# Performance work log

Hardware: AMD Instinct MI355X
Metric: run time of the kernel (lower is better)

Reference implementation:

```python
import jax, jax.numpy as jnp
import numpy as np

# Config (matches init_kwargs)
L = 2        # depth
DIM = 512
H = 8        # heads
DH = 64      # dim_head
MLP = 2048
B = 4
N = 1024
BLOCK = 32   # compress / selection block size
TOPK = 8     # num_selected_blocks
WRAD = 32    # sliding window radius (window size 64)


def setup_inputs() -> dict:
    key = jax.random.key(0)
    ks = jax.random.split(key, 10)
    s = 0.02
    def rn(k, shape):
        return jax.random.normal(k, shape, dtype=jnp.float32) * s
    return {
        "x": jax.random.normal(ks[0], (B, N, DIM), dtype=jnp.float32),
        "ln1_g": jnp.ones((L, DIM), jnp.float32), "ln1_b": jnp.zeros((L, DIM), jnp.float32),
        "Wq": rn(ks[1], (L, DIM, H * DH)), "Wk": rn(ks[2], (L, DIM, H * DH)), "Wv": rn(ks[3], (L, DIM, H * DH)),
        "Wg": rn(ks[4], (L, DIM, H * 3)), "bg": jnp.zeros((L, H * 3), jnp.float32),
        "Wo": rn(ks[5], (L, H * DH, DIM)), "bo": jnp.zeros((L, DIM), jnp.float32),
        "ln2_g": jnp.ones((L, DIM), jnp.float32), "ln2_b": jnp.zeros((L, DIM), jnp.float32),
        "W1": rn(ks[6], (L, DIM, MLP)), "b1": jnp.zeros((L, MLP), jnp.float32),
        "W2": rn(ks[7], (L, MLP, DIM)), "b2": jnp.zeros((L, DIM), jnp.float32),
    }


def _ln(x, g, b):
    m = x.mean(-1, keepdims=True)
    v = jnp.var(x, axis=-1, keepdims=True)
    return (x - m) * jax.lax.rsqrt(v + 1e-5) * g + b


def _sparse_attn(x, lng, lnb, Wq, Wk, Wv, Wg, bg, Wo, bo):
    # NSA-style 3-branch attention: compressed + selected-blocks + sliding window,
    # combined with per-head sigmoid gates. Non-causal (ViT).
    b, n, _ = x.shape
    h = _ln(x, lng, lnb)
    q = (h @ Wq).reshape(b, n, H, DH).transpose(0, 2, 1, 3)  # bhnd
    k = (h @ Wk).reshape(b, n, H, DH).transpose(0, 2, 1, 3)
    v = (h @ Wv).reshape(b, n, H, DH).transpose(0, 2, 1, 3)
    q = q * (DH ** -0.5)
    nb = n // BLOCK
    # --- compressed branch: mean-pool K/V per block
    kc = k.reshape(b, H, nb, BLOCK, DH).mean(3)              # bhmd (m = nb blocks)
    vc = v.reshape(b, H, nb, BLOCK, DH).mean(3)
    sc = jnp.einsum('bhnd,bhmd->bhnm', q, kc)                # per-query block scores
    out_c = jnp.einsum('bhnm,bhmd->bhnd', jax.nn.softmax(sc, -1), vc)
    # --- selection branch: top-k blocks per query (from compressed scores)
    idx = jax.lax.top_k(sc, TOPK)[1]                         # [b,h,n,TOPK]
    blk_mask = (idx[..., :, None] == jnp.arange(nb)).any(-2) # [b,h,n,nb]
    tok_mask = jnp.repeat(blk_mask, BLOCK, axis=-1)          # [b,h,n,n]
    s = jnp.einsum('bhnd,bhmd->bhnm', q, k)                  # shared fine scores
    neg = jnp.finfo(s.dtype).min
    out_s = jnp.einsum('bhnm,bhmd->bhnd',
                       jax.nn.softmax(jnp.where(tok_mask, s, neg), -1), v)
    # --- sliding window branch
    i = jnp.arange(n)
    wmask = jnp.abs(i[:, None] - i[None, :]) <= WRAD
    out_w = jnp.einsum('bhnm,bhmd->bhnd',
                       jax.nn.softmax(jnp.where(wmask, s, neg), -1), v)
    # --- gate and combine
    gates = jax.nn.sigmoid(h @ Wg + bg).reshape(b, n, H, 3).transpose(0, 2, 1, 3)[..., None]  # [b,H,n,3,1]
    out = gates[:, :, :, 0] * out_c + gates[:, :, :, 1] * out_s + gates[:, :, :, 2] * out_w
    out = out.transpose(0, 2, 1, 3).reshape(b, n, H * DH)
    return out @ Wo + bo


def reference(x, ln1_g, ln1_b, Wq, Wk, Wv, Wg, bg, Wo, bo, ln2_g, ln2_b, W1, b1, W2, b2):
    for l in range(L):
        x = _sparse_attn(x, ln1_g[l], ln1_b[l], Wq[l], Wk[l], Wv[l],
                         Wg[l], bg[l], Wo[l], bo[l]) + x
        h = _ln(x, ln2_g[l], ln2_b[l])
        x = jax.nn.gelu(h @ W1[l] + b1[l]) @ W2[l] + b2[l] + x
    return x
```

## Files before the change

### kernel.cpp

```cpp
#include <hip/hip_runtime.h>
#include <cstdint>
#include <cstddef>

typedef __attribute__((ext_vector_type(4))) float f32x4;
typedef __attribute__((ext_vector_type(16))) float f32x16;
typedef __attribute__((ext_vector_type(8))) short short8;
typedef __attribute__((ext_vector_type(4))) short s16x4;
typedef __attribute__((ext_vector_type(2))) int int2v;
typedef unsigned short u16;

#define DEVINL static __device__ __forceinline__
#define MFMA32(A,B,C) __builtin_amdgcn_mfma_f32_32x32x16_bf16(A,B,C,0,0,0)

constexpr int NBATCH = 4;
constexpr int NSEQ   = 1024;
constexpr int NDIM   = 512;
constexpr int NHEAD  = 8;
constexpr int NDH    = 64;
constexpr int NMLP   = 2048;
constexpr int NROWS  = NBATCH * NSEQ;
constexpr int NBLKC  = 32;
constexpr int NBH    = NBATCH * NHEAD;
constexpr int NQKV   = 1664;

DEVINL float b2f(u16 u) { union { unsigned u; float f; } x; x.u = ((unsigned)u) << 16; return x.f; }
DEVINL u16 f2b(float v) {
    union { float f; unsigned u; } x; x.f = v;
    unsigned r = x.u + 0x7fff + ((x.u >> 16) & 1);
    return (u16)(r >> 16);
}
DEVINL float fastrcp(float x) { float r; asm("v_rcp_f32 %0, %1" : "=v"(r) : "v"(x)); return r; }

DEVINL void gload16(const void* g, void* l)
{
    __builtin_amdgcn_global_load_lds(
        (const __attribute__((address_space(1))) void*)g,
        (__attribute__((address_space(3))) void*)l, 16, 0, 0);
}

__global__ void __launch_bounds__(256) ln_kernel(const float* __restrict__ x,
    const float* __restrict__ gg, const float* __restrict__ bb, u16* __restrict__ out)
{
    int row = blockIdx.x * 4 + (threadIdx.x >> 6);
    int lane = threadIdx.x & 63;
    const float* xr = x + (size_t)row * NDIM + lane * 8;
    f32x4 a = *(const f32x4*)xr;
    f32x4 c = *(const f32x4*)(xr + 4);
    float xv[8] = { a[0], a[1], a[2], a[3], c[0], c[1], c[2], c[3] };
    float s = 0.f, s2 = 0.f;
    #pragma unroll
    for (int i = 0; i < 8; ++i) { s += xv[i]; s2 += xv[i] * xv[i]; }
    #pragma unroll
    for (int d = 1; d < 64; d <<= 1) { s += __shfl_xor(s, d); s2 += __shfl_xor(s2, d); }
    float mean = s * (1.f / NDIM);
    float var = s2 * (1.f / NDIM) - mean * mean;
    float rstd = rsqrtf(var + 1e-5f);
    const float* gp = gg + lane * 8;
    const float* bp = bb + lane * 8;
    short8 o;
    #pragma unroll
    for (int i = 0; i < 8; ++i)
        o[i] = (short)f2b((xv[i] - mean) * rstd * gp[i] + bp[i]);
    *(short8*)(out + (size_t)row * NDIM + lane * 8) = o;
}

__global__ void __launch_bounds__(256) transpose_w(const float* __restrict__ W,
    u16* __restrict__ WT, int K, int Nc, size_t sstr, size_t dstr)
{
    W  += (size_t)blockIdx.z * sstr;
    WT += (size_t)blockIdx.z * dstr;
    __shared__ float tile[32][33];
    int tx = threadIdx.x & 31;
    int ty = threadIdx.x >> 5;
    int n0 = blockIdx.x * 32, k0 = blockIdx.y * 32;
    #pragma unroll
    for (int r = 0; r < 4; ++r) {
        int kr = ty * 4 + r;
        tile[kr][tx] = W[(size_t)(k0 + kr) * Nc + n0 + tx];
    }
    __syncthreads();
    #pragma unroll
    for (int r = 0; r < 4; ++r) {
        int nr = ty * 4 + r;
        WT[(size_t)(n0 + nr) * K + k0 + tx] = f2b(tile[tx][nr]);
    }
}

__global__ void __launch_bounds__(256) transpose_qkv(const float* __restrict__ Wq,
    const float* __restrict__ Wk, const float* __restrict__ Wv, u16* __restrict__ WT)
{
    int z = blockIdx.z;
    int l = z / 3, w = z % 3;
    const float* W = (w == 0 ? Wq : (w == 1 ? Wk : Wv)) + (size_t)l * 262144;
    u16* dst = WT + (size_t)l * NQKV * 512 + (size_t)w * 512 * 512;
    __shared__ float tile[32][33];
    int tx = threadIdx.x & 31;
    int ty = threadIdx.x >> 5;
    int n0 = blockIdx.x * 32, k0 = blockIdx.y * 32;
    #pragma unroll
    for (int r = 0; r < 4; ++r) {
        int kr = ty * 4 + r;
        tile[kr][tx] = W[(size_t)(k0 + kr) * 512 + n0 + tx];
    }
    __syncthreads();
    #pragma unroll
    for (int r = 0; r < 4; ++r) {
        int nr = ty * 4 + r;
        dst[(size_t)(n0 + nr) * 512 + k0 + tx] = f2b(tile[tx][nr]);
    }
}

__global__ void __launch_bounds__(256) fill_wg(const float* __restrict__ Wg, u16* __restrict__ WT)
{
    int l = blockIdx.x, r = blockIdx.y;
    u16* dst = WT + (size_t)l * NQKV * 512 + (size_t)(1536 + r) * 512;
    const float* src = Wg + (size_t)l * 512 * 24;
    for (int k = threadIdx.x; k < 512; k += 256)
        dst[k] = (r < 24) ? f2b(src[(size_t)k * 24 + r]) : (u16)0;
}

__global__ void __launch_bounds__(256) pool_kernel(const u16* __restrict__ kb,
    const u16* __restrict__ vt, u16* __restrict__ kc16, u16* __restrict__ vct16)
{
    int idx = blockIdx.x * 256 + threadIdx.x;
    int d = idx & 63, m = (idx >> 6) & 31, bh = idx >> 11;
    const u16* kp = kb + ((size_t)bh * NSEQ + m * 32) * NDH + d;
    float sk = 0.f;
    #pragma unroll 8
    for (int j = 0; j < 32; ++j) sk += b2f(kp[j * NDH]);
    const u16* vp = vt + (size_t)bh * 65536 + (size_t)d * NSEQ + m * 32;
    float sv = 0.f;
    #pragma unroll 8
    for (int j = 0; j < 32; ++j) sv += b2f(vp[j]);
    kc16[(size_t)bh * 2048 + m * 64 + d] = f2b(sk * (1.f / 32.f));
    vct16[(size_t)bh * 2048 + d * 32 + m] = f2b(sv * (1.f / 32.f));
}

enum { EP_QKV = 0, EP_GELU = 1, EP_RES = 2 };

template<int BM, int BN, int BK, int KT, int EPIL>
__global__ void __launch_bounds__(256) gemm_k(
    const u16* __restrict__ A, const u16* __restrict__ BT,
    int M, int Nc,
    const float* __restrict__ bias,
    float* __restrict__ resout,
    u16* __restrict__ outb,
    u16* __restrict__ q16, u16* __restrict__ k16, u16* __restrict__ vt16)
{
    constexpr int NT = KT / BK;
    constexpr int NK = BK / 32;
    constexpr int RB = BK * 2;
    constexpr int RMSK = (BK == 64) ? 7 : 3;
    constexpr int LA = BM * BK / 2048;
    constexpr int LBD = BN * BK / 2048;
    constexpr int LB = LA + LBD;
    constexpr int WM = BM / 2, WN = BN / 2;
    constexpr int MI = WM / 16, NI = WN / 16;
    __shared__ u16 As[3][BM][BK];
    __shared__ u16 Bs[3][BN][BK];
    const int tid = threadIdx.x;
    const int lane = tid & 63;
    const int wid = tid >> 6;
    const int wm = wid >> 1, wn = wid & 1;
    const int gx = gridDim.x;
    const int nblk = gx * gridDim.y;
    const int id = blockIdx.y * gx + blockIdx.x;
    const int sid = (id & 7) * (nblk >> 3) + (id >> 3);
    const int rowBase = (sid / gx) * BM;
    const int colBase = (sid % gx) * BN;
    const int fr = lane & 15;
    const int kg = lane >> 4;

    auto stage = [&](int buf, int t) {
        const size_t k0 = (size_t)t * BK;
        char* aL = (char*)&As[buf][0][0];
        #pragma unroll
        for (int p = 0; p < LA; ++p) {
            int idx = p * 256 + tid;
            int row = idx / (BK / 8);
            int ob = (idx % (BK / 8)) * 16;
            int sw = ob ^ ((row & RMSK) << 4);
            gload16((const char*)(A + (size_t)(rowBase + row) * KT + k0) + sw, aL + idx * 16);
        }
        char* bL = (char*)&Bs[buf][0][0];
        #pragma unroll
        for (int p = 0; p < LBD; ++p) {
            int idx = p * 256 + tid;
            int row = idx / (BK / 8);
            int ob = (idx % (BK / 8)) * 16;
            int sw = ob ^ ((row & RMSK) << 4);
            gload16((const char*)(BT + (size_t)(colBase + row) * KT + k0) + sw, bL + idx * 16);
        }
    };

    stage(0, 0);
    stage(1, 1);
    f32x4 acc[MI][NI] = {};
    int cb = 0, nb = 1, sb = 2;
    for (int t = 0; t < NT; ++t) {
        if (t == NT - 1) asm volatile("s_waitcnt vmcnt(0)" ::: "memory");
        else             asm volatile("s_waitcnt vmcnt(%0)" :: "n"(LB) : "memory");
        __builtin_amdgcn_s_barrier();
        if (t + 2 < NT) stage(sb, t + 2);
        const char* aB = (const char*)&As[cb][0][0];
        const char* bB = (const char*)&Bs[cb][0][0];
        #pragma unroll
        for (int kk = 0; kk < NK; ++kk) {
            short8 af[MI], bfr[NI];
            #pragma unroll
            for (int i = 0; i < MI; ++i) {
                int row = wm * WM + i * 16 + fr;
                af[i] = *(const short8*)(aB + row * RB + ((kk * 64 + kg * 16) ^ ((row & RMSK) << 4)));
            }
            #pragma unroll
            for (int j = 0; j < NI; ++j) {
                int row = wn * WN + j * 16 + fr;
                bfr[j] = *(const short8*)(bB + row * RB + ((kk * 64 + kg * 16) ^ ((row & RMSK) << 4)));
            }
            #pragma unroll
            for (int i = 0; i < MI; ++i)
                #pragma unroll
                for (int j = 0; j < NI; ++j)
                    acc[i][j] = __builtin_amdgcn_mfma_f32_16x16x32_bf16(af[i], bfr[j], acc[i][j], 0, 0, 0);
        }
        int tmp = cb; cb = nb; nb = sb; sb = tmp;
    }

    #pragma unroll
    for (int i = 0; i < MI; ++i) {
        #pragma unroll
        for (int j = 0; j < NI; ++j) {
            int col = colBase + wn * WN + j * 16 + fr;
            if constexpr (EPIL == EP_QKV) {
                int which = col >> 9;
                int row0 = rowBase + wm * WM + i * 16 + kg * 4;
                if (which >= 3) {
                    int c2 = col - 1536;
                    if (c2 < 24) {
                        #pragma unroll
                        for (int rr = 0; rr < 4; ++rr) {
                            float xg = acc[i][j][rr] + bias[c2];
                            resout[(size_t)(row0 + rr) * 24 + c2] =
                                fastrcp(1.f + exp2f(-1.4426950409f * xg));
                        }
                    }
                } else {
                    int c = col & 511;
                    int hh = c >> 6, dh = c & 63;
                    int bb2 = row0 >> 10, n0 = row0 & 1023;
                    size_t bh2 = (size_t)(bb2 * NHEAD + hh) * 65536;
                    if (which == 2) {
                        s16x4 pk;
                        #pragma unroll
                        for (int rr = 0; rr < 4; ++rr) pk[rr] = (short)f2b(acc[i][j][rr]);
                        *(s16x4*)&vt16[bh2 + (size_t)dh * NSEQ + n0] = pk;
                    } else {
                        u16* dst = (which ? k16 : q16) + bh2 + (size_t)n0 * NDH + dh;
                        float scl = which ? 1.f : 0.18033688f;
                        #pragma unroll
                        for (int rr = 0; rr < 4; ++rr) dst[rr * NDH] = f2b(acc[i][j][rr] * scl);
                    }
                }
            } else {
                #pragma unroll
                for (int rr = 0; rr < 4; ++rr) {
                    int row = rowBase + wm * WM + i * 16 + kg * 4 + rr;
                    float val = acc[i][j][rr];
                    if constexpr (EPIL == EP_GELU) {
                        float t = val + bias[col];
                        float u = t + 0.044715f * t * t * t;
                        float gs = fastrcp(1.f + exp2f(-2.3022083f * u));
                        outb[(size_t)row * Nc + col] = f2b(t * gs);
                    } else {
                        resout[(size_t)row * Nc + col] += val + bias[col];
                    }
                }
            }
        }
    }
}

DEVINL unsigned cvtpk(float lo, float hi_)
{
    unsigned t;
    asm("v_cvt_pk_bf16_f32 %0, %1, %2" : "=v"(t) : "v"(lo), "v"(hi_));
    return t;
}

DEVINL void plswap(unsigned& a, unsigned& b)
{
#if __has_builtin(__builtin_amdgcn_permlane32_swap)
    int2v r = __builtin_amdgcn_permlane32_swap((int)a, (int)b, false, false);
    a = (unsigned)r[0]; b = (unsigned)r[1];
#else
    asm("v_permlane32_swap_b32 %0, %1" : "+v"(a), "+v"(b));
#endif
}

DEVINL void packswap(const float* e, unsigned selmask, short8& pb0, short8& pb1)
{
    unsigned w[8];
    #pragma unroll
    for (int i = 0; i < 8; ++i) w[i] = cvtpk(e[2 * i], e[2 * i + 1]) & selmask;
    plswap(w[0], w[2]); plswap(w[1], w[3]);
    plswap(w[4], w[6]); plswap(w[5], w[7]);
    union { unsigned u[4]; short8 s; } c0, c1;
    c0.u[0] = w[0]; c0.u[1] = w[1]; c0.u[2] = w[2]; c0.u[3] = w[3];
    c1.u[0] = w[4]; c1.u[1] = w[5]; c1.u[2] = w[6]; c1.u[3] = w[7];
    pb0 = c0.s; pb1 = c1.s;
}

template<int R0>
DEVINL unsigned rank4(const f32x16& sc_, const float* po, int hi)
{
    unsigned bits = 0;
    #pragma unroll
    for (int k = 0; k < 4; ++k) {
        const int r = R0 + k;
        const int krr = (r & 3) + 8 * (r >> 2);
        const float sr = sc_[r];
        int cnt = 0;
        #pragma unroll
        for (int j = 0; j < 16; ++j) {
            const int krj = (j & 3) + 8 * (j >> 2);
            if (j != r) cnt += (sc_[j] > sr || (sc_[j] == sr && krj < krr)) ? 1 : 0;
            const bool pless = (hi == 0) ? (krj + 4 < krr) : (krj < krr + 4);
            cnt += (po[j] > sr || (po[j] == sr && pless)) ? 1 : 0;
        }
        if (cnt < 8) bits |= 1u << (krr + 4 * hi);
    }
    return bits;
}

__global__ void __launch_bounds__(256, 2) attn_mfma(
    const u16* __restrict__ qb, const u16* __restrict__ kb, const u16* __restrict__ vt,
    const u16* __restrict__ kc16, const u16* __restrict__ vct16,
    const float* __restrict__ gates, u16* __restrict__ att)
{
    __shared__ __align__(16) char smem[65536];
    unsigned* selb_lds = (unsigned*)(smem + 32768);
    const int tid = threadIdx.x;
    const int wid = tid >> 6;
    const int lane = tid & 63;
    const int qc = lane & 31, hi = lane >> 5;
    const int g = blockIdx.x;
    const int xcd = g & 7, ii = g >> 3;
    const int bh = xcd * 4 + (ii >> 5);
    const int qt = ii & 31;
    const int qrow = qt * 32 + qc;
    if (tid < 32) selb_lds[tid] = 0u;
    const u16* Q = qb + (size_t)bh * 65536;
    const char* Kby = (const char*)(kb + (size_t)bh * 65536);
    const char* Vby = (const char*)(vt + (size_t)bh * 65536);

    const int l16 = lane * 16;
    auto stage = [&](int buf, int blk) {
        char* base = smem + buf * 32768 + wid * 4096;
        #pragma unroll
        for (int i = 0; i < 4; ++i) {
            int o = i * 1024 + l16;
            int so = o ^ (((o >> 7) & 7) << 4);
            gload16(Kby + (size_t)blk * 4096 + so, base + o);
        }
        #pragma unroll
        for (int i = 0; i < 4; ++i) {
            int o = i * 1024 + l16;
            int row = o >> 6;
            int colb = (o & 63) ^ ((row & 3) << 4);
            gload16(Vby + (size_t)row * 2048 + blk * 64 + colb, base + 16384 + o);
        }
    };
    const int blo = wid * 8;
    stage(0, blo);

    short8 qf[4];
    #pragma unroll
    for (int ks = 0; ks < 4; ++ks)
        qf[ks] = *(const short8*)&Q[(size_t)qrow * 64 + ks * 16 + hi * 8];
    const int b = bh >> 3, h = bh & 7;
    const float* grow = gates + (size_t)(b * 1024 + qrow) * 24 + h * 3;
    const float g0 = grow[0], g1 = grow[1], g2 = grow[2];

    const u16* Kc = kc16 + (size_t)bh * 2048;
    const u16* Vc = vct16 + (size_t)bh * 2048;
    f32x16 sc_ = {};
    #pragma unroll
    for (int ks = 0; ks < 4; ++ks) {
        short8 kcf = *(const short8*)&Kc[qc * 64 + ks * 16 + hi * 8];
        sc_ = MFMA32(kcf, qf[ks], sc_);
    }
    float po[16];
    #pragma unroll
    for (int r = 0; r < 16; ++r) po[r] = __shfl_xor(sc_[r], 32);
    unsigned bits;
    switch (wid) {
        case 0:  bits = rank4<0>(sc_, po, hi); break;
        case 1:  bits = rank4<4>(sc_, po, hi); break;
        case 2:  bits = rank4<8>(sc_, po, hi); break;
        default: bits = rank4<12>(sc_, po, hi); break;
    }
    __syncthreads();
    atomicOr(&selb_lds[qc], bits);

    f32x16 aC = {};
    float denc = 1.f;
    if (wid < 2) {
        float ec[16]; float dsum = 0.f;
        #pragma unroll
        for (int r = 0; r < 16; ++r) { ec[r] = exp2f(sc_[r]); dsum += ec[r]; }
        denc = dsum + __shfl_xor(dsum, 32);
        short8 pc0, pc1;
        packswap(ec, 0xFFFFFFFFu, pc0, pc1);
        const u16* Vch = Vc + (wid * 32 + qc) * 32 + hi * 8;
        short8 vcA = *(const short8*)&Vch[0];
        short8 vcB = *(const short8*)&Vch[16];
        aC = MFMA32(vcA, pc0, aC);
        aC = MFMA32(vcB, pc1, aC);
    }
    __syncthreads();
    const unsigned mask = selb_lds[qc];

    f32x16 aS0 = {}, aS1 = {}, aW0 = {}, aW1 = {};
    float denS = 0.f, denW = 0.f;
    const int wlo = qt > 0 ? qt - 1 : 0;
    const int whi = qt < 31 ? qt + 1 : 31;

    int kra[4];
    #pragma unroll
    for (int ks = 0; ks < 4; ++ks)
        kra[ks] = wid * 4096 + ((qc * 128 + ks * 32 + hi * 16) ^ ((qc & 7) << 4));
    const int vbase = wid * 4096 + 16384;
    const int v00o = vbase + ((qc * 64 + hi * 16) ^ ((qc & 3) << 4));
    const int v01o = vbase + ((qc * 64 + 32 + hi * 16) ^ ((qc & 3) << 4));
    const int v10o = vbase + ((2048 + qc * 64 + hi * 16) ^ ((qc & 3) << 4));
    const int v11o = vbase + ((2048 + qc * 64 + 32 + hi * 16) ^ ((qc & 3) << 4));

    for (int t = 0; t < 8; ++t) {
        const int blk = blo + t;
        const char* base = smem + (t & 1) * 32768;
        if (t < 7) {
            stage((t + 1) & 1, blk + 1);
            asm volatile("s_waitcnt vmcnt(8)" ::: "memory");
        } else {
            asm volatile("s_waitcnt vmcnt(0)" ::: "memory");
        }
        short8 kf[4];
        #pragma unroll
        for (int ks = 0; ks < 4; ++ks)
            kf[ks] = *(const short8*)(base + kra[ks]);
        __builtin_amdgcn_s_setprio(1);
        f32x16 s = {};
        #pragma unroll
        for (int ks = 0; ks < 4; ++ks)
            s = MFMA32(kf[ks], qf[ks], s);
        __builtin_amdgcn_s_setprio(0);
        float e[16];
        #pragma unroll
        for (int r = 0; r < 16; ++r) e[r] = exp2f(s[r]);

        short8 v00 = *(const short8*)(base + v00o);
        short8 v01 = *(const short8*)(base + v01o);
        short8 v10 = *(const short8*)(base + v10o);
        short8 v11 = *(const short8*)(base + v11o);

        const bool selb = (mask >> blk) & 1u;
        const unsigned selm = selb ? 0xFFFFFFFFu : 0u;
        {
            float tt = 0.f;
            #pragma unroll
            for (int r = 0; r < 16; ++r) tt += e[r];
            denS += selb ? tt : 0.f;
        }
        short8 pb0, pb1;
        packswap(e, selm, pb0, pb1);
        __builtin_amdgcn_s_setprio(1);
        aS0 = MFMA32(v00, pb0, aS0);
        aS0 = MFMA32(v01, pb1, aS0);
        aS1 = MFMA32(v10, pb0, aS1);
        aS1 = MFMA32(v11, pb1, aS1);
        __builtin_amdgcn_s_setprio(0);

        if (blk >= wlo && blk <= whi) {
            float ew[16];
            float tt = 0.f;
            #pragma unroll
            for (int r = 0; r < 16; ++r) {
                int kr = (r & 3) + 8 * (r >> 2) + 4 * hi;
                int dd = blk * 32 + kr - qrow;
                ew[r] = (dd >= -32 && dd <= 32) ? e[r] : 0.f;
                tt += ew[r];
            }
            denW += tt;
            short8 pw0, pw1;
            packswap(ew, 0xFFFFFFFFu, pw0, pw1);
            aW0 = MFMA32(v00, pw0, aW0);
            aW0 = MFMA32(v01, pw1, aW0);
            aW1 = MFMA32(v10, pw0, aW1);
            aW1 = MFMA32(v11, pw1, aW1);
        }
    }
    __syncthreads();

    float* cmb = (float*)smem;
    if (wid > 0) {
        float* dst = cmb + (size_t)(wid - 1) * (64 * 85) + lane * 85;
        #pragma unroll
        for (int i = 0; i < 16; ++i) { dst[i] = aS0[i]; dst[16 + i] = aS1[i]; }
        #pragma unroll
        for (int i = 0; i < 16; ++i) { dst[32 + i] = aW0[i]; dst[48 + i] = aW1[i]; }
        dst[64] = denS; dst[65] = denW;
        if (wid == 1) {
            #pragma unroll
            for (int i = 0; i < 16; ++i) dst[66 + i] = aC[i];
        }
    }
    __syncthreads();
    if (wid == 0) {
        #pragma unroll
        for (int w = 1; w < 4; ++w) {
            const float* src = cmb + (size_t)(w - 1) * (64 * 85) + lane * 85;
            #pragma unroll
            for (int i = 0; i < 16; ++i) { aS0[i] += src[i]; aS1[i] += src[16 + i]; }
            #pragma unroll
            for (int i = 0; i < 16; ++i) { aW0[i] += src[32 + i]; aW1[i] += src[48 + i]; }
            denS += src[64]; denW += src[65];
        }
        f32x16 aC1;
        const float* s1 = cmb + lane * 85;
        #pragma unroll
        for (int i = 0; i < 16; ++i) aC1[i] = s1[66 + i];
        denS += __shfl_xor(denS, 32);
        denW += __shfl_xor(denW, 32);
        const float rc = g0 / denc, rs = g1 / denS, rw = g2 / denW;
        u16* op = att + (size_t)(b * 1024 + qrow) * NDIM + h * 64;
        #pragma unroll
        for (int c4 = 0; c4 < 4; ++c4) {
            int d0 = c4 * 8 + hi * 4;
            s16x4 w0, w1;
            #pragma unroll
            for (int j = 0; j < 4; ++j) {
                w0[j] = (short)f2b(rc * aC[c4 * 4 + j]  + rs * aS0[c4 * 4 + j] + rw * aW0[c4 * 4 + j]);
                w1[j] = (short)f2b(rc * aC1[c4 * 4 + j] + rs * aS1[c4 * 4 + j] + rw * aW1[c4 * 4 + j]);
            }
            *(s16x4*)&op[d0] = w0;
            *(s16x4*)&op[d0 + 32] = w1;
        }
    }
}

extern "C" void kernel_launch(void* const* d_in, const int* in_sizes, int n_in,
                              void* d_out, int out_size, void* d_ws, size_t ws_size,
                              hipStream_t stream)
{
    const float* x0    = (const float*)d_in[0];
    const float* ln1_g = (const float*)d_in[1];
    const float* ln1_b = (const float*)d_in[2];
    const float* Wq    = (const float*)d_in[3];
    const float* Wk    = (const float*)d_in[4];
    const float* Wv    = (const float*)d_in[5];
    const float* Wg    = (const float*)d_in[6];
    const float* bg    = (const float*)d_in[7];
    const float* Wo    = (const float*)d_in[8];
    const float* bo    = (const float*)d_in[9];
    const float* ln2_g = (const float*)d_in[10];
    const float* ln2_b = (const float*)d_in[11];
    const float* W1    = (const float*)d_in[12];
    const float* b1    = (const float*)d_in[13];
    const float* W2    = (const float*)d_in[14];
    const float* b2    = (const float*)d_in[15];
    float* xo = (float*)d_out;

    char* w = (char*)d_ws;
    auto alloc = [&](size_t bytes) { char* p = w; w += (bytes + 255) & ~(size_t)255; return p; };
    u16*   hbf   = (u16*)  alloc((size_t)NROWS * NDIM * 2);
    u16*   qb    = (u16*)  alloc((size_t)NBH * NSEQ * NDH * 2);
    u16*   kb    = (u16*)  alloc((size_t)NBH * NSEQ * NDH * 2);
    u16*   vt    = (u16*)  alloc((size_t)NBH * NDH * NSEQ * 2);
    u16*   att   = (u16*)  alloc((size_t)NROWS * NDIM * 2);
    float* gates = (float*)alloc((size_t)NROWS * NHEAD * 3 * 4);
    u16*   kc16  = (u16*)  alloc((size_t)NBH * NBLKC * NDH * 2);
    u16*   vct16 = (u16*)  alloc((size_t)NBH * NDH * NBLKC * 2);
    u16*   wqkvT = (u16*)  alloc((size_t)2 * NQKV * 512 * 2);
    u16*   woT   = (u16*)  alloc((size_t)2 * 512 * 512 * 2);
    u16*   w1T   = (u16*)  alloc((size_t)2 * 2048 * 512 * 2);
    u16*   w2T   = (u16*)  alloc((size_t)2 * 512 * 2048 * 2);
    u16*   mid   = (u16*)qb;

    hipMemcpyAsync(xo, x0, (size_t)NROWS * NDIM * 4, hipMemcpyDeviceToDevice, stream);

    transpose_qkv<<<dim3(16, 16, 6), 256, 0, stream>>>(Wq, Wk, Wv, wqkvT);
    fill_wg<<<dim3(2, 128), 256, 0, stream>>>(Wg, wqkvT);
    transpose_w<<<dim3(16, 16, 2), 256, 0, stream>>>(Wo, woT, 512, 512,  262144, 262144);
    transpose_w<<<dim3(64, 16, 2), 256, 0, stream>>>(W1, w1T, 512, 2048, 1048576, 1048576);
    transpose_w<<<dim3(16, 64, 2), 256, 0, stream>>>(W2, w2T, 2048, 512, 1048576, 1048576);

    for (int l = 0; l < 2; ++l) {
        ln_kernel<<<NROWS / 4, 256, 0, stream>>>(xo, ln1_g + l * NDIM, ln1_b + l * NDIM, hbf);
        gemm_k<64, 128, 64, 512, EP_QKV><<<dim3(NQKV / 128, NROWS / 64), 256, 0, stream>>>(
            hbf, wqkvT + (size_t)l * NQKV * 512, NROWS, NQKV,
            bg + l * 24, gates, nullptr, qb, kb, vt);
        pool_kernel<<<(NBH * NBLKC * NDH) / 256, 256, 0, stream>>>(kb, vt, kc16, vct16);
        attn_mfma<<<1024, 256, 0, stream>>>(qb, kb, vt, kc16, vct16, gates, att);
        gemm_k<64, 64, 64, 512, EP_RES><<<dim3(512 / 64, NROWS / 64), 256, 0, stream>>>(
            att, woT + (size_t)l * 512 * 512, NROWS, 512,
            bo + l * NDIM, xo, nullptr, nullptr, nullptr, nullptr);
        ln_kernel<<<NROWS / 4, 256, 0, stream>>>(xo, ln2_g + l * NDIM, ln2_b + l * NDIM, hbf);
        gemm_k<64, 128, 64, 512, EP_GELU><<<dim3(2048 / 128, NROWS / 64), 256, 0, stream>>>(
            hbf, w1T + (size_t)l * 2048 * 512, NROWS, 2048,
            b1 + l * NMLP, nullptr, mid, nullptr, nullptr, nullptr);
        gemm_k<64, 64, 64, 2048, EP_RES><<<dim3(512 / 64, NROWS / 64), 256, 0, stream>>>(
            mid, w2T + (size_t)l * 512 * 2048, NROWS, 512,
            b2 + l * NDIM, xo, nullptr, nullptr, nullptr, nullptr);
    }
}
```

Measured before the change: 246.8 us.

## Merge weight-prep kernels and restructure attention for higher occupancy with smaller LDS

Folds the five weight transpose/fill launches into one setup_weights kernel to cut launch overhead. The attention kernel halves its LDS (single-buffered staging) and raises launch bounds to 4 blocks per CU. The sliding-window branch moves to its own per-wave stage, and the compressed-score MFMA is recomputed later rather than kept live. The cross-wave reduction is now serialized through a swizzled LDS buffer, which adds barriers and gives up the double-buffered load/compute overlap in exchange for occupancy.

```diff
diff --git a/kernel.cpp b/kernel.cpp
--- a/kernel.cpp
+++ b/kernel.cpp
@@ -64,59 +64,53 @@
     *(short8*)(out + (size_t)row * NDIM + lane * 8) = o;
 }
 
-__global__ void __launch_bounds__(256) transpose_w(const float* __restrict__ W,
-    u16* __restrict__ WT, int K, int Nc, size_t sstr, size_t dstr)
-{
-    W  += (size_t)blockIdx.z * sstr;
-    WT += (size_t)blockIdx.z * dstr;
+__global__ void __launch_bounds__(256) setup_weights(
+    const float* __restrict__ Wq, const float* __restrict__ Wk, const float* __restrict__ Wv,
+    const float* __restrict__ Wg, const float* __restrict__ Wo,
+    const float* __restrict__ W1, const float* __restrict__ W2,
+    u16* __restrict__ wqkvT, u16* __restrict__ woT,
+    u16* __restrict__ w1T, u16* __restrict__ w2T)
+{
+    int j = blockIdx.x;
+    if (j >= 6144) {
+        int j5 = j - 6144, l = j5 >> 2, chunk = j5 & 3;
+        u16* d2 = wqkvT + (size_t)l * NQKV * 512 + (size_t)(1536 + chunk * 32) * 512;
+        const float* src = Wg + (size_t)l * 512 * 24;
+        for (int e = threadIdx.x; e < 16384; e += 256) {
+            int r = chunk * 32 + (e >> 9), k = e & 511;
+            d2[(size_t)(e >> 9) * 512 + k] = (r < 24) ? f2b(src[(size_t)k * 24 + r]) : (u16)0;
+        }
+        return;
+    }
     __shared__ float tile[32][33];
-    int tx = threadIdx.x & 31;
-    int ty = threadIdx.x >> 5;
-    int n0 = blockIdx.x * 32, k0 = blockIdx.y * 32;
-    #pragma unroll
-    for (int r = 0; r < 4; ++r) {
-        int kr = ty * 4 + r;
-        tile[kr][tx] = W[(size_t)(k0 + kr) * Nc + n0 + tx];
-    }
+    const float* W; u16* dst; int K, Nc, bx, by;
+    if (j < 1536) {
+        int z = j >> 8, t = j & 255, l = z / 3, wsel = z % 3;
+        W = (wsel == 0 ? Wq : (wsel == 1 ? Wk : Wv)) + (size_t)l * 262144;
+        dst = wqkvT + (size_t)l * NQKV * 512 + (size_t)wsel * 262144;
+        K = 512; Nc = 512; bx = t & 15; by = t >> 4;
+    } else if (j < 2048) {
+        int j2 = j - 1536, z = j2 >> 8, t = j2 & 255;
+        W = Wo + (size_t)z * 262144; dst = woT + (size_t)z * 262144;
+        K = 512; Nc = 512; bx = t & 15; by = t >> 4;
+    } else if (j < 4096) {
+        int j3 = j - 2048, z = j3 >> 10, t = j3 & 1023;
+        W = W1 + (size_t)z * 1048576; dst = w1T + (size_t)z * 1048576;
+        K = 512; Nc = 2048; bx = t & 63; by = t >> 6;
+    } else {
+        int j4 = j - 4096, z = j4 >> 10, t = j4 & 1023;
+        W = W2 + (size_t)z * 1048576; dst = w2T + (size_t)z * 1048576;
+        K = 2048; Nc = 512; bx = t & 15; by = t >> 4;
+    }
+    int tx = threadIdx.x & 31, ty = threadIdx.x >> 5;
+    int n0 = bx * 32, k0 = by * 32;
+    #pragma unroll
+    for (int r = 0; r < 4; ++r)
+        tile[ty * 4 + r][tx] = W[(size_t)(k0 + ty * 4 + r) * Nc + n0 + tx];
     __syncthreads();
     #pragma unroll
-    for (int r = 0; r < 4; ++r) {
-        int nr = ty * 4 + r;
-        WT[(size_t)(n0 + nr) * K + k0 + tx] = f2b(tile[tx][nr]);
-    }
-}
-
-__global__ void __launch_bounds__(256) transpose_qkv(const float* __restrict__ Wq,
-    const float* __restrict__ Wk, const float* __restrict__ Wv, u16* __restrict__ WT)
-{
-    int z = blockIdx.z;
-    int l = z / 3, w = z % 3;
-    const float* W = (w == 0 ? Wq : (w == 1 ? Wk : Wv)) + (size_t)l * 262144;
-    u16* dst = WT + (size_t)l * NQKV * 512 + (size_t)w * 512 * 512;
-    __shared__ float tile[32][33];
-    int tx = threadIdx.x & 31;
-    int ty = threadIdx.x >> 5;
-    int n0 = blockIdx.x * 32, k0 = blockIdx.y * 32;
-    #pragma unroll
-    for (int r = 0; r < 4; ++r) {
-        int kr = ty * 4 + r;
-        tile[kr][tx] = W[(size_t)(k0 + kr) * 512 + n0 + tx];
-    }
-    __syncthreads();
-    #pragma unroll
-    for (int r = 0; r < 4; ++r) {
-        int nr = ty * 4 + r;
-        dst[(size_t)(n0 + nr) * 512 + k0 + tx] = f2b(tile[tx][nr]);
-    }
-}
-
-__global__ void __launch_bounds__(256) fill_wg(const float* __restrict__ Wg, u16* __restrict__ WT)
-{
-    int l = blockIdx.x, r = blockIdx.y;
-    u16* dst = WT + (size_t)l * NQKV * 512 + (size_t)(1536 + r) * 512;
-    const float* src = Wg + (size_t)l * 512 * 24;
-    for (int k = threadIdx.x; k < 512; k += 256)
-        dst[k] = (r < 24) ? f2b(src[(size_t)k * 24 + r]) : (u16)0;
+    for (int r = 0; r < 4; ++r)
+        dst[(size_t)(n0 + ty * 4 + r) * K + k0 + tx] = f2b(tile[tx][ty * 4 + r]);
 }
 
 __global__ void __launch_bounds__(256) pool_kernel(const u16* __restrict__ kb,
@@ -332,17 +326,18 @@
     return bits;
 }
 
-__global__ void __launch_bounds__(256, 2) attn_mfma(
+__global__ void __launch_bounds__(256, 4) attn_mfma(
     const u16* __restrict__ qb, const u16* __restrict__ kb, const u16* __restrict__ vt,
     const u16* __restrict__ kc16, const u16* __restrict__ vct16,
     const float* __restrict__ gates, u16* __restrict__ att)
 {
-    __shared__ __align__(16) char smem[65536];
-    unsigned* selb_lds = (unsigned*)(smem + 32768);
+    __shared__ __align__(16) char smem[32768];
+    __shared__ unsigned selb_lds[32];
     const int tid = threadIdx.x;
     const int wid = tid >> 6;
     const int lane = tid & 63;
     const int qc = lane & 31, hi = lane >> 5;
+    const int lm = lane & 31;
     const int g = blockIdx.x;
     const int xcd = g & 7, ii = g >> 3;
     const int bh = xcd * 4 + (ii >> 5);
@@ -354,8 +349,8 @@
     const char* Vby = (const char*)(vt + (size_t)bh * 65536);
 
     const int l16 = lane * 16;
-    auto stage = [&](int buf, int blk) {
-        char* base = smem + buf * 32768 + wid * 4096;
+    auto stage = [&](int blk) {
+        char* base = smem + wid * 8192;
         #pragma unroll
         for (int i = 0; i < 4; ++i) {
             int o = i * 1024 + l16;
@@ -367,11 +362,11 @@
             int o = i * 1024 + l16;
             int row = o >> 6;
             int colb = (o & 63) ^ ((row & 3) << 4);
-            gload16(Vby + (size_t)row * 2048 + blk * 64 + colb, base + 16384 + o);
+            gload16(Vby + (size_t)row * 2048 + blk * 64 + colb, base + 4096 + o);
         }
     };
     const int blo = wid * 8;
-    stage(0, blo);
+    stage(blo);
 
     short8 qf[4];
     #pragma unroll
@@ -383,31 +378,134 @@
 
     const u16* Kc = kc16 + (size_t)bh * 2048;
     const u16* Vc = vct16 + (size_t)bh * 2048;
-    f32x16 sc_ = {};
-    #pragma unroll
-    for (int ks = 0; ks < 4; ++ks) {
-        short8 kcf = *(const short8*)&Kc[qc * 64 + ks * 16 + hi * 8];
-        sc_ = MFMA32(kcf, qf[ks], sc_);
-    }
-    float po[16];
-    #pragma unroll
-    for (int r = 0; r < 16; ++r) po[r] = __shfl_xor(sc_[r], 32);
-    unsigned bits;
-    switch (wid) {
-        case 0:  bits = rank4<0>(sc_, po, hi); break;
-        case 1:  bits = rank4<4>(sc_, po, hi); break;
-        case 2:  bits = rank4<8>(sc_, po, hi); break;
-        default: bits = rank4<12>(sc_, po, hi); break;
-    }
-    __syncthreads();
-    atomicOr(&selb_lds[qc], bits);
+    {
+        f32x16 sc_ = {};
+        #pragma unroll
+        for (int ks = 0; ks < 4; ++ks) {
+            short8 kcf = *(const short8*)&Kc[qc * 64 + ks * 16 + hi * 8];
+            sc_ = MFMA32(kcf, qf[ks], sc_);
+        }
+        float po[16];
+        #pragma unroll
+        for (int r = 0; r < 16; ++r) po[r] = __shfl_xor(sc_[r], 32);
+        unsigned bits;
+        switch (wid) {
+            case 0:  bits = rank4<0>(sc_, po, hi); break;
+            case 1:  bits = rank4<4>(sc_, po, hi); break;
+            case 2:  bits = rank4<8>(sc_, po, hi); break;
+            default: bits = rank4<12>(sc_, po, hi); break;
+        }
+        __syncthreads();
+        atomicOr(&selb_lds[qc], bits);
+        __syncthreads();
+    }
+    const unsigned mask = selb_lds[qc];
+
+    int kra[4];
+    #pragma unroll
+    for (int ks = 0; ks < 4; ++ks)
+        kra[ks] = wid * 8192 + ((qc * 128 + ks * 32 + hi * 16) ^ ((qc & 7) << 4));
+    const int vbase = wid * 8192 + 4096;
+    const int v00o = vbase + ((qc * 64 + hi * 16) ^ ((qc & 3) << 4));
+    const int v01o = vbase + ((qc * 64 + 32 + hi * 16) ^ ((qc & 3) << 4));
+    const int v10o = vbase + ((2048 + qc * 64 + hi * 16) ^ ((qc & 3) << 4));
+    const int v11o = vbase + ((2048 + qc * 64 + 32 + hi * 16) ^ ((qc & 3) << 4));
+    const char* base = smem;
+
+    f32x16 aS0 = {}, aS1 = {};
+    float denS = 0.f;
+    for (int t = 0; t < 8; ++t) {
+        const int blk = blo + t;
+        asm volatile("s_waitcnt vmcnt(0)" ::: "memory");
+        short8 kf[4];
+        #pragma unroll
+        for (int ks = 0; ks < 4; ++ks)
+            kf[ks] = *(const short8*)(base + kra[ks]);
+        short8 v00 = *(const short8*)(base + v00o);
+        short8 v01 = *(const short8*)(base + v01o);
+        short8 v10 = *(const short8*)(base + v10o);
+        short8 v11 = *(const short8*)(base + v11o);
+        if (t < 7) {
+            asm volatile("s_waitcnt lgkmcnt(0)" ::: "memory");
+            stage(blk + 1);
+        }
+        __builtin_amdgcn_s_setprio(1);
+        f32x16 s = {};
+        #pragma unroll
+        for (int ks = 0; ks < 4; ++ks)
+            s = MFMA32(kf[ks], qf[ks], s);
+        __builtin_amdgcn_s_setprio(0);
+        float e[16];
+        #pragma unroll
+        for (int r = 0; r < 16; ++r) e[r] = exp2f(s[r]);
+        const bool selb = (mask >> blk) & 1u;
+        const unsigned selm = selb ? 0xFFFFFFFFu : 0u;
+        {
+            float tt = 0.f;
+            #pragma unroll
+            for (int r = 0; r < 16; ++r) tt += e[r];
+            denS += selb ? tt : 0.f;
+        }
+        short8 pb0, pb1;
+        packswap(e, selm, pb0, pb1);
+        __builtin_amdgcn_s_setprio(1);
+        aS0 = MFMA32(v00, pb0, aS0);
+        aS0 = MFMA32(v01, pb1, aS0);
+        aS1 = MFMA32(v10, pb0, aS1);
+        aS1 = MFMA32(v11, pb1, aS1);
+        __builtin_amdgcn_s_setprio(0);
+    }
+
+    f32x16 aW0 = {}, aW1 = {};
+    float denW = 0.f;
+    const int wblk = qt - 1 + wid;
+    if (wid < 3 && wblk >= 0 && wblk <= 31) {
+        asm volatile("s_waitcnt lgkmcnt(0)" ::: "memory");
+        stage(wblk);
+        asm volatile("s_waitcnt vmcnt(0)" ::: "memory");
+        short8 kf[4];
+        #pragma unroll
+        for (int ks = 0; ks < 4; ++ks)
+            kf[ks] = *(const short8*)(base + kra[ks]);
+        short8 v00 = *(const short8*)(base + v00o);
+        short8 v01 = *(const short8*)(base + v01o);
+        short8 v10 = *(const short8*)(base + v10o);
+        short8 v11 = *(const short8*)(base + v11o);
+        f32x16 s = {};
+        #pragma unroll
+        for (int ks = 0; ks < 4; ++ks)
+            s = MFMA32(kf[ks], qf[ks], s);
+        float ew[16];
+        float tt = 0.f;
+        #pragma unroll
+        for (int r = 0; r < 16; ++r) {
+            int kr = (r & 3) + 8 * (r >> 2) + 4 * hi;
+            int dd = wblk * 32 + kr - qrow;
+            float ev = exp2f(s[r]);
+            ew[r] = (dd >= -32 && dd <= 32) ? ev : 0.f;
+            tt += ew[r];
+        }
+        denW += tt;
+        short8 pw0, pw1;
+        packswap(ew, 0xFFFFFFFFu, pw0, pw1);
+        aW0 = MFMA32(v00, pw0, aW0);
+        aW0 = MFMA32(v01, pw1, aW0);
+        aW1 = MFMA32(v10, pw0, aW1);
+        aW1 = MFMA32(v11, pw1, aW1);
+    }
 
     f32x16 aC = {};
     float denc = 1.f;
     if (wid < 2) {
+        f32x16 sc2 = {};
+        #pragma unroll
+        for (int ks = 0; ks < 4; ++ks) {
+            short8 kcf = *(const short8*)&Kc[qc * 64 + ks * 16 + hi * 8];
+            sc2 = MFMA32(kcf, qf[ks], sc2);
+        }
         float ec[16]; float dsum = 0.f;
         #pragma unroll
-        for (int r = 0; r < 16; ++r) { ec[r] = exp2f(sc_[r]); dsum += ec[r]; }
+        for (int r = 0; r < 16; ++r) { ec[r] = exp2f(sc2[r]); dsum += ec[r]; }
         denc = dsum + __shfl_xor(dsum, 32);
         short8 pc0, pc1;
         packswap(ec, 0xFFFFFFFFu, pc0, pc1);
@@ -417,118 +515,48 @@
         aC = MFMA32(vcA, pc0, aC);
         aC = MFMA32(vcB, pc1, aC);
     }
+
     __syncthreads();
-    const unsigned mask = selb_lds[qc];
-
-    f32x16 aS0 = {}, aS1 = {}, aW0 = {}, aW1 = {};
-    float denS = 0.f, denW = 0.f;
-    const int wlo = qt > 0 ? qt - 1 : 0;
-    const int whi = qt < 31 ? qt + 1 : 31;
-
-    int kra[4];
-    #pragma unroll
-    for (int ks = 0; ks < 4; ++ks)
-        kra[ks] = wid * 4096 + ((qc * 128 + ks * 32 + hi * 16) ^ ((qc & 7) << 4));
-    const int vbase = wid * 4096 + 16384;
-    const int v00o = vbase + ((qc * 64 + hi * 16) ^ ((qc & 3) << 4));
-    const int v01o = vbase + ((qc * 64 + 32 + hi * 16) ^ ((qc & 3) << 4));
-    const int v10o = vbase + ((2048 + qc * 64 + hi * 16) ^ ((qc & 3) << 4));
-    const int v11o = vbase + ((2048 + qc * 64 + 32 + hi * 16) ^ ((qc & 3) << 4));
-
-    for (int t = 0; t < 8; ++t) {
-        const int blk = blo + t;
-        const char* base = smem + (t & 1) * 32768;
-        if (t < 7) {
-            stage((t + 1) & 1, blk + 1);
-            asm volatile("s_waitcnt vmcnt(8)" ::: "memory");
-        } else {
-            asm volatile("s_waitcnt vmcnt(0)" ::: "memory");
-        }
-        short8 kf[4];
-        #pragma unroll
-        for (int ks = 0; ks < 4; ++ks)
-            kf[ks] = *(const short8*)(base + kra[ks]);
-        __builtin_amdgcn_s_setprio(1);
-        f32x16 s = {};
-        #pragma unroll
-        for (int ks = 0; ks < 4; ++ks)
-            s = MFMA32(kf[ks], qf[ks], s);
-        __builtin_amdgcn_s_setprio(0);
-        float e[16];
-        #pragma unroll
-        for (int r = 0; r < 16; ++r) e[r] = exp2f(s[r]);
-
-        short8 v00 = *(const short8*)(base + v00o);
-        short8 v01 = *(const short8*)(base + v01o);
-        short8 v10 = *(const short8*)(base + v10o);
-        short8 v11 = *(const short8*)(base + v11o);
-
-        const bool selb = (mask >> blk) & 1u;
-        const unsigned selm = selb ? 0xFFFFFFFFu : 0u;
-        {
-            float tt = 0.f;
+    float* pay = (float*)smem;
+    f32x16 aC1 = {};
+    #define SW(s) (((s) & ~31) | (((s) & 31) ^ lm))
+    for (int w = 1; w < 4; ++w) {
+        if (wid == w) {
+            float* d = pay + (size_t)lane * 128;
             #pragma unroll
-            for (int r = 0; r < 16; ++r) tt += e[r];
-            denS += selb ? tt : 0.f;
-        }
-        short8 pb0, pb1;
-        packswap(e, selm, pb0, pb1);
-        __builtin_amdgcn_s_setprio(1);
-        aS0 = MFMA32(v00, pb0, aS0);
-        aS0 = MFMA32(v01, pb1, aS0);
-        aS1 = MFMA32(v10, pb0, aS1);
-        aS1 = MFMA32(v11, pb1, aS1);
-        __builtin_amdgcn_s_setprio(0);
-
-        if (blk >= wlo && blk <= whi) {
-            float ew[16];
-            float tt = 0.f;
+            for (int i = 0; i < 16; ++i) { d[SW(i)] = aS0[i]; d[SW(16 + i)] = aS1[i]; }
+            if (w < 3) {
+                #pragma unroll
+                for (int i = 0; i < 16; ++i) { d[SW(32 + i)] = aW0[i]; d[SW(48 + i)] = aW1[i]; }
+                d[97] = denW;
+            }
+            if (w == 1) {
+                #pragma unroll
+                for (int i = 0; i < 16; ++i) d[SW(64 + i)] = aC[i];
+            }
+            d[96] = denS;
+        }
+        __syncthreads();
+        if (wid == 0) {
+            const float* sr = pay + (size_t)lane * 128;
             #pragma unroll
-            for (int r = 0; r < 16; ++r) {
-                int kr = (r & 3) + 8 * (r >> 2) + 4 * hi;
-                int dd = blk * 32 + kr - qrow;
-                ew[r] = (dd >= -32 && dd <= 32) ? e[r] : 0.f;
-                tt += ew[r];
-            }
-            denW += tt;
-            short8 pw0, pw1;
-            packswap(ew, 0xFFFFFFFFu, pw0, pw1);
-            aW0 = MFMA32(v00, pw0, aW0);
-            aW0 = MFMA32(v01, pw1, aW0);
-            aW1 = MFMA32(v10, pw0, aW1);
-            aW1 = MFMA32(v11, pw1, aW1);
-        }
-    }
-    __syncthreads();
-
-    float* cmb = (float*)smem;
-    if (wid > 0) {
-        float* dst = cmb + (size_t)(wid - 1) * (64 * 85) + lane * 85;
-        #pragma unroll
-        for (int i = 0; i < 16; ++i) { dst[i] = aS0[i]; dst[16 + i] = aS1[i]; }
-        #pragma unroll
-        for (int i = 0; i < 16; ++i) { dst[32 + i] = aW0[i]; dst[48 + i] = aW1[i]; }
-        dst[64] = denS; dst[65] = denW;
-        if (wid == 1) {
-            #pragma unroll
-            for (int i = 0; i < 16; ++i) dst[66 + i] = aC[i];
-        }
-    }
-    __syncthreads();
+            for (int i = 0; i < 16; ++i) { aS0[i] += sr[SW(i)]; aS1[i] += sr[SW(16 + i)]; }
+            denS += sr[96];
+            if (w < 3) {
+                #pragma unroll
+                for (int i = 0; i < 16; ++i) { aW0[i] += sr[SW(32 + i)]; aW1[i] += sr[SW(48 + i)]; }
+                denW += sr[97];
+            }
+            if (w == 1) {
+                #pragma unroll
+                for (int i = 0; i < 16; ++i) aC1[i] = sr[SW(64 + i)];
+            }
+        }
+        __syncthreads();
+    }
+    #undef SW
+
     if (wid == 0) {
-        #pragma unroll
-        for (int w = 1; w < 4; ++w) {
-            const float* src = cmb + (size_t)(w - 1) * (64 * 85) + lane * 85;
-            #pragma unroll
-            for (int i = 0; i < 16; ++i) { aS0[i] += src[i]; aS1[i] += src[16 + i]; }
-            #pragma unroll
-            for (int i = 0; i < 16; ++i) { aW0[i] += src[32 + i]; aW1[i] += src[48 + i]; }
-            denS += src[64]; denW += src[65];
-        }
-        f32x16 aC1;
-        const float* s1 = cmb + lane * 85;
-        #pragma unroll
-        for (int i = 0; i < 16; ++i) aC1[i] = s1[66 + i];
         denS += __shfl_xor(denS, 32);
         denW += __shfl_xor(denW, 32);
         const float rc = g0 / denc, rs = g1 / denS, rw = g2 / denW;
@@ -588,11 +616,7 @@
 
     hipMemcpyAsync(xo, x0, (size_t)NROWS * NDIM * 4, hipMemcpyDeviceToDevice, stream);
 
-    transpose_qkv<<<dim3(16, 16, 6), 256, 0, stream>>>(Wq, Wk, Wv, wqkvT);
-    fill_wg<<<dim3(2, 128), 256, 0, stream>>>(Wg, wqkvT);
-    transpose_w<<<dim3(16, 16, 2), 256, 0, stream>>>(Wo, woT, 512, 512,  262144, 262144);
-    transpose_w<<<dim3(64, 16, 2), 256, 0, stream>>>(W1, w1T, 512, 2048, 1048576, 1048576);
-    transpose_w<<<dim3(16, 64, 2), 256, 0, stream>>>(W2, w2T, 2048, 512, 1048576, 1048576);
+    setup_weights<<<6152, 256, 0, stream>>>(Wq, Wk, Wv, Wg, Wo, W1, W2, wqkvT, woT, w1T, w2T);
 
     for (int l = 0; l < 2; ++l) {
         ln_kernel<<<NROWS / 4, 256, 0, stream>>>(xo, ln1_g + l * NDIM, ln1_b + l * NDIM, hbf);
```

Result: slower. 544.5 us (+120.6%).
